# Kernel optimization log

Hardware: AMD Instinct MI355X
Metric: run time of the kernel (lower is better)

## Reference

```python
import jax, jax.numpy as jnp
import numpy as np
from jax import lax

T, D, H, O = 16384, 257, 512, 257


def setup_inputs() -> dict:
    key = jax.random.key(0)
    ks = jax.random.split(key, 7)
    s = 1.0 / np.sqrt(H)  # PyTorch LSTM/Linear uniform init scale
    u = lambda k, shp: jax.random.uniform(k, shp, jnp.float32, -s, s)
    return {
        "stft": jax.random.normal(ks[0], (T, D), jnp.float32),
        "W_ih": u(ks[1], (4 * H, D)),
        "W_hh": u(ks[2], (4 * H, H)),
        "b_ih": u(ks[3], (4 * H,)),
        "b_hh": u(ks[4], (4 * H,)),
        "W_out": u(ks[5], (O, H)),
        "b_out": u(ks[6], (O,)),
    }


def reference(stft, W_ih, W_hh, b_ih, b_hh, W_out, b_out):
    # Batch size is 1 (stft.view(T, 1, -1)), so we scan over [T, D] directly.
    # Precompute input-to-gate GEMM for all timesteps: [T, 4H]
    x_gates = stft @ W_ih.T + (b_ih + b_hh)

    def step(carry, xg):
        h, c = carry  # [H], [H]
        g = xg + h @ W_hh.T  # [4H], PyTorch gate order: i, f, g, o
        i, f, gg, o = jnp.split(g, 4)
        i = jax.nn.sigmoid(i)
        f = jax.nn.sigmoid(f)
        gg = jnp.tanh(gg)
        o = jax.nn.sigmoid(o)
        c = f * c + i * gg
        h = o * jnp.tanh(c)
        return (h, c), h

    h0 = jnp.zeros((H,), stft.dtype)  # init_hidden(): zeros
    c0 = jnp.zeros((H,), stft.dtype)
    _, hs = lax.scan(step, (h0, c0), x_gates)  # hs: [T, H]

    out_space = hs @ W_out.T + b_out  # [T, O]
    return jax.nn.log_softmax(out_space, axis=1)
```

## Files before the change

### kernel.cpp

```cpp
#include <hip/hip_runtime.h>
#include <cmath>

#define T_STEPS 16384
#define D_IN    257
#define H_DIM   512
#define O_DIM   257
#define G4      2048

typedef unsigned long long u64;

#define WS_XG_OFF     8192
#define WS_HS_OFF     (8192 + (size_t)T_STEPS * G4 * 4)

__device__ inline float fast_sigmoid(float x) {
    return 1.f / (1.f + __expf(-x));
}
__device__ inline float fast_tanh(float x) {
    float ax = fminf(fabsf(x), 15.f);
    float e  = __expf(2.f * ax);
    float t  = (e - 1.f) / (e + 1.f);
    return copysignf(t, x);
}
__device__ inline float dot4(float4 a, float4 b) {
    return a.x * b.x + a.y * b.y + a.z * b.z + a.w * b.w;
}

__global__ __launch_bounds__(256) void xgate_gemm(
    const float* __restrict__ stft, const float* __restrict__ W_ih,
    const float* __restrict__ b_ih, const float* __restrict__ b_hh,
    float* __restrict__ xg)
{
    const int tid = threadIdx.x;
    const int tx = tid & 15, ty = tid >> 4;
    const int j0 = blockIdx.x * 64;
    const int t0 = blockIdx.y * 64;

    __shared__ float s_a[64][17];
    __shared__ float s_b[64][17];

    float acc[4][4] = {};

    for (int k0 = 0; k0 < D_IN; k0 += 16) {
        #pragma unroll
        for (int l = 0; l < 4; ++l) {
            int idx = tid + l * 256;
            int r  = idx >> 4;
            int kk = idx & 15;
            int k  = k0 + kk;
            s_a[r][kk] = (k < D_IN) ? stft[(size_t)(t0 + r) * D_IN + k] : 0.f;
            s_b[r][kk] = (k < D_IN) ? W_ih[(size_t)(j0 + r) * D_IN + k] : 0.f;
        }
        __syncthreads();
        #pragma unroll
        for (int kk = 0; kk < 16; ++kk) {
            float a[4], b[4];
            #pragma unroll
            for (int r = 0; r < 4; ++r) a[r] = s_a[ty * 4 + r][kk];
            #pragma unroll
            for (int c = 0; c < 4; ++c) b[c] = s_b[tx * 4 + c][kk];
            #pragma unroll
            for (int r = 0; r < 4; ++r)
                #pragma unroll
                for (int c = 0; c < 4; ++c)
                    acc[r][c] += a[r] * b[c];
        }
        __syncthreads();
    }

    float bias[4];
    #pragma unroll
    for (int c = 0; c < 4; ++c) {
        int j = j0 + tx * 4 + c;
        bias[c] = b_ih[j] + b_hh[j];
    }
    #pragma unroll
    for (int r = 0; r < 4; ++r) {
        int t = t0 + ty * 4 + r;
        #pragma unroll
        for (int c = 0; c < 4; ++c) {
            xg[(size_t)t * G4 + j0 + tx * 4 + c] = acc[r][c] + bias[c];
        }
    }
}

__global__ __launch_bounds__(512, 1) void lstm_seq(
    const float* __restrict__ W_hh, const float* __restrict__ xg,
    float* __restrict__ hs, u64* msg)
{
    const int tid  = threadIdx.x;
    const int g    = blockIdx.x;
    const int w    = tid >> 6;
    const int lane = tid & 63;
    const int j    = lane >> 2;
    const int c    = lane & 3;
    const int colb = w * 64 + c * 16;

    const float* wbase = W_hh + (size_t)(g * 16 + j) * H_DIM + colb;
    const size_t gstride = (size_t)H_DIM * H_DIM;
    float4 wA0, wA1, wA2, wA3, wB0, wB1, wB2, wB3;
    float4 wC0, wC1, wC2, wC3, wD0, wD1, wD2, wD3;
    {
        const float4* p0 = (const float4*)(wbase);
        const float4* p1 = (const float4*)(wbase + gstride);
        const float4* p2 = (const float4*)(wbase + 2 * gstride);
        const float4* p3 = (const float4*)(wbase + 3 * gstride);
        wA0 = p0[0]; wA1 = p0[1]; wA2 = p0[2]; wA3 = p0[3];
        wB0 = p1[0]; wB1 = p1[1]; wB2 = p1[2]; wB3 = p1[3];
        wC0 = p2[0]; wC1 = p2[1]; wC2 = p2[2]; wC3 = p2[3];
        wD0 = p3[0]; wD1 = p3[1]; wD2 = p3[2]; wD3 = p3[3];
    }

    __shared__ float s_h[512];
    __shared__ float s_part[2][512];

    u64* slot0 = msg;
    u64* slot1 = msg + 512;

    float c_state = 0.f;

    const int t_j    = lane & 15;

    for (int t = 0; t < T_STEPS; ++t) {
        const unsigned tagt = (unsigned)t;

        float xv = 0.f;
        if (w == 0) xv = xg[(size_t)t * G4 + (lane >> 4) * H_DIM + g * 16 + t_j];

        u64* rp = ((t & 1) ? slot1 : slot0) + tid;
        u64 u;
        for (;;) {
            u = __hip_atomic_load(rp, __ATOMIC_RELAXED, __HIP_MEMORY_SCOPE_AGENT);
            if ((unsigned)(u >> 32) == tagt) break;
        }

        s_h[tid] = __uint_as_float((unsigned)u);

        const float4* hv = (const float4*)(s_h + colb);
        float4 h0 = hv[0], h1 = hv[1], h2 = hv[2], h3 = hv[3];

        float p0 = dot4(wA0, h0) + dot4(wA1, h1) + dot4(wA2, h2) + dot4(wA3, h3);
        float p1 = dot4(wB0, h0) + dot4(wB1, h1) + dot4(wB2, h2) + dot4(wB3, h3);
        float p2 = dot4(wC0, h0) + dot4(wC1, h1) + dot4(wC2, h2) + dot4(wC3, h3);
        float p3 = dot4(wD0, h0) + dot4(wD1, h1) + dot4(wD2, h2) + dot4(wD3, h3);

        const bool lo2 = (c < 2);
        float a0 = (lo2 ? p0 : p2) + __shfl_xor(lo2 ? p2 : p0, 2, 64);
        float a1 = (lo2 ? p1 : p3) + __shfl_xor(lo2 ? p3 : p1, 2, 64);
        const bool ev = ((c & 1) == 0);
        float fin = (ev ? a0 : a1) + __shfl_xor(ev ? a1 : a0, 1, 64);

        s_part[t & 1][w * 64 + c * 16 + j] = fin;

        asm volatile("s_waitcnt lgkmcnt(0)\n\ts_barrier" ::: "memory");

        if (w == 0) {
            const float* pp = &s_part[t & 1][0];
            float sum = xv;
            #pragma unroll
            for (int k = 0; k < 8; ++k) sum += pp[k * 64 + lane];

            float gi = __shfl(sum, t_j + 0,  64);
            float gf = __shfl(sum, t_j + 16, 64);
            float gg = __shfl(sum, t_j + 32, 64);
            float go = __shfl(sum, t_j + 48, 64);

            float iv = fast_sigmoid(gi);
            float fv = fast_sigmoid(gf);
            float ov = fast_sigmoid(go);
            float gv = fast_tanh(gg);
            c_state = fv * c_state + iv * gv;
            float hn = ov * fast_tanh(c_state);

            if (lane < 16) {
                hs[(size_t)t * H_DIM + g * 16 + lane] = hn;
                u64 m = ((u64)(tagt + 1) << 32) | (u64)__float_as_uint(hn);
                u64* wp = (((t + 1) & 1) ? slot1 : slot0) + (g * 16 + lane);
                __hip_atomic_store(wp, m, __ATOMIC_RELAXED, __HIP_MEMORY_SCOPE_AGENT);
            }
        }
    }
}

__global__ __launch_bounds__(256) void out_softmax(
    const float* __restrict__ hs, const float* __restrict__ W_out,
    const float* __restrict__ b_out, float* __restrict__ out)
{
    const int tid = threadIdx.x;
    const int t0  = blockIdx.x * 16;

    __shared__ float s_w[257 * 33];
    __shared__ float s_hs[16 * 33];
    __shared__ float s_o[16 * 257];
    __shared__ float s_red[8];

    float acc[16] = {};
    float acc256 = 0.f;

    for (int k0 = 0; k0 < H_DIM; k0 += 32) {
        for (int idx = tid; idx < 257 * 32; idx += 256) {
            int row = idx >> 5, col = idx & 31;
            s_w[row * 33 + col] = W_out[(size_t)row * H_DIM + k0 + col];
        }
        for (int idx = tid; idx < 16 * 32; idx += 256) {
            int row = idx >> 5, col = idx & 31;
            s_hs[row * 33 + col] = hs[(size_t)(t0 + row) * H_DIM + k0 + col];
        }
        __syncthreads();
        #pragma unroll
        for (int kk = 0; kk < 32; ++kk) {
            float w = s_w[tid * 33 + kk];
            #pragma unroll
            for (int r = 0; r < 16; ++r)
                acc[r] += s_hs[r * 33 + kk] * w;
        }
        if (tid < 16) {
            #pragma unroll
            for (int kk = 0; kk < 32; ++kk)
                acc256 += s_w[256 * 33 + kk] * s_hs[tid * 33 + kk];
        }
        __syncthreads();
    }

    float bias_c = b_out[tid];
    #pragma unroll
    for (int r = 0; r < 16; ++r) s_o[r * 257 + tid] = acc[r] + bias_c;
    if (tid < 16) s_o[tid * 257 + 256] = acc256 + b_out[256];
    __syncthreads();

    const int lane = tid & 63, wid = tid >> 6;
    for (int r = 0; r < 16; ++r) {
        float v  = s_o[r * 257 + tid];
        float vx = (tid == 0) ? s_o[r * 257 + 256] : -INFINITY;
        float m = fmaxf(v, vx);
        #pragma unroll
        for (int off = 32; off > 0; off >>= 1) m = fmaxf(m, __shfl_xor(m, off, 64));
        if (lane == 0) s_red[wid] = m;
        __syncthreads();
        m = fmaxf(fmaxf(s_red[0], s_red[1]), fmaxf(s_red[2], s_red[3]));
        float e = expf(v - m) + ((tid == 0) ? expf(vx - m) : 0.f);
        #pragma unroll
        for (int off = 32; off > 0; off >>= 1) e += __shfl_xor(e, off, 64);
        if (lane == 0) s_red[4 + wid] = e;
        __syncthreads();
        float s = s_red[4] + s_red[5] + s_red[6] + s_red[7];
        float lg = logf(s) + m;
        out[(size_t)(t0 + r) * O_DIM + tid] = v - lg;
        if (tid == 0) out[(size_t)(t0 + r) * O_DIM + 256] = vx - lg;
    }
}

extern "C" void kernel_launch(void* const* d_in, const int* in_sizes, int n_in,
                              void* d_out, int out_size, void* d_ws, size_t ws_size,
                              hipStream_t stream) {
    (void)in_sizes; (void)n_in; (void)out_size; (void)ws_size;

    const float* stft  = (const float*)d_in[0];
    const float* W_ih  = (const float*)d_in[1];
    const float* W_hh  = (const float*)d_in[2];
    const float* b_ih  = (const float*)d_in[3];
    const float* b_hh  = (const float*)d_in[4];
    const float* W_out = (const float*)d_in[5];
    const float* b_out = (const float*)d_in[6];
    float* out = (float*)d_out;

    char* ws = (char*)d_ws;
    u64* msg  = (u64*)ws;
    float* xg = (float*)(ws + WS_XG_OFF);
    float* hs = (float*)(ws + WS_HS_OFF);

    (void)hipMemsetAsync(ws, 0, 8192, stream);

    xgate_gemm<<<dim3(G4 / 64, T_STEPS / 64), 256, 0, stream>>>(
        stft, W_ih, b_ih, b_hh, xg);
    lstm_seq<<<32, 512, 0, stream>>>(W_hh, xg, hs, msg);
    out_softmax<<<T_STEPS / 16, 256, 0, stream>>>(hs, W_out, b_out, out);
}
```

Before: 27.47 ms.

## Spread LSTM gate epilogue across all warps and prefetch next h message

The post-barrier gate reduction and activation work, previously done by wave 0 alone, is now split across all 8 waves. Each wave reduces partials for 2 hidden units with xor-shuffles and publishes them. A speculative load of the next step's message slot is issued early, so the spin-wait can often finish without a fresh round trip. This shortens the serial critical path per timestep but adds more publishing threads and extra xg loads per wave.

```diff
diff --git a/kernel.cpp b/kernel.cpp
--- a/kernel.cpp
+++ b/kernel.cpp
@@ -116,24 +116,32 @@
     u64* slot0 = msg;
     u64* slot1 = msg + 512;
 
-    float c_state = 0.f;
-
-    const int t_j    = lane & 15;
+    const int rr    = lane >> 3;
+    const int gateT = rr >> 1;
+    const int hhT   = rr & 1;
+    const int rowT  = gateT * 16 + 2 * w + hhT;
+
+    float c_st0 = 0.f, c_st1 = 0.f;
+
+    u64 u_spec = __hip_atomic_load(slot0 + tid, __ATOMIC_RELAXED,
+                                   __HIP_MEMORY_SCOPE_AGENT);
 
     for (int t = 0; t < T_STEPS; ++t) {
         const unsigned tagt = (unsigned)t;
-
-        float xv = 0.f;
-        if (w == 0) xv = xg[(size_t)t * G4 + (lane >> 4) * H_DIM + g * 16 + t_j];
-
-        u64* rp = ((t & 1) ? slot1 : slot0) + tid;
-        u64 u;
-        for (;;) {
+        const int buf = t & 1;
+
+        float xv = xg[(size_t)t * G4 + gateT * H_DIM + g * 16 + 2 * w + hhT];
+
+        u64* rp = (buf ? slot1 : slot0) + tid;
+        u64 u = u_spec;
+        while ((unsigned)(u >> 32) != tagt) {
             u = __hip_atomic_load(rp, __ATOMIC_RELAXED, __HIP_MEMORY_SCOPE_AGENT);
-            if ((unsigned)(u >> 32) == tagt) break;
         }
 
         s_h[tid] = __uint_as_float((unsigned)u);
+
+        u_spec = __hip_atomic_load(((buf ^ 1) ? slot1 : slot0) + tid,
+                                   __ATOMIC_RELAXED, __HIP_MEMORY_SCOPE_AGENT);
 
         const float4* hv = (const float4*)(s_h + colb);
         float4 h0 = hv[0], h1 = hv[1], h2 = hv[2], h3 = hv[3];
@@ -149,34 +157,37 @@
         const bool ev = ((c & 1) == 0);
         float fin = (ev ? a0 : a1) + __shfl_xor(ev ? a1 : a0, 1, 64);
 
-        s_part[t & 1][w * 64 + c * 16 + j] = fin;
+        s_part[buf][w * 64 + c * 16 + j] = fin;
 
         asm volatile("s_waitcnt lgkmcnt(0)\n\ts_barrier" ::: "memory");
 
-        if (w == 0) {
-            const float* pp = &s_part[t & 1][0];
-            float sum = xv;
-            #pragma unroll
-            for (int k = 0; k < 8; ++k) sum += pp[k * 64 + lane];
-
-            float gi = __shfl(sum, t_j + 0,  64);
-            float gf = __shfl(sum, t_j + 16, 64);
-            float gg = __shfl(sum, t_j + 32, 64);
-            float go = __shfl(sum, t_j + 48, 64);
-
-            float iv = fast_sigmoid(gi);
-            float fv = fast_sigmoid(gf);
-            float ov = fast_sigmoid(go);
-            float gv = fast_tanh(gg);
-            c_state = fv * c_state + iv * gv;
-            float hn = ov * fast_tanh(c_state);
-
-            if (lane < 16) {
-                hs[(size_t)t * H_DIM + g * 16 + lane] = hn;
-                u64 m = ((u64)(tagt + 1) << 32) | (u64)__float_as_uint(hn);
-                u64* wp = (((t + 1) & 1) ? slot1 : slot0) + (g * 16 + lane);
-                __hip_atomic_store(wp, m, __ATOMIC_RELAXED, __HIP_MEMORY_SCOPE_AGENT);
-            }
+        float sum = s_part[buf][(lane & 7) * 64 + rowT];
+        sum += __shfl_xor(sum, 1, 64);
+        sum += __shfl_xor(sum, 2, 64);
+        sum += __shfl_xor(sum, 4, 64);
+        float total = sum + xv;
+
+        float gi0 = __shfl(total, 0,  64), gi1 = __shfl(total, 8,  64);
+        float gf0 = __shfl(total, 16, 64), gf1 = __shfl(total, 24, 64);
+        float gg0 = __shfl(total, 32, 64), gg1 = __shfl(total, 40, 64);
+        float go0 = __shfl(total, 48, 64), go1 = __shfl(total, 56, 64);
+
+        float iv0 = fast_sigmoid(gi0), iv1 = fast_sigmoid(gi1);
+        float fv0 = fast_sigmoid(gf0), fv1 = fast_sigmoid(gf1);
+        float ov0 = fast_sigmoid(go0), ov1 = fast_sigmoid(go1);
+        float gv0 = fast_tanh(gg0),    gv1 = fast_tanh(gg1);
+        c_st0 = fv0 * c_st0 + iv0 * gv0;
+        c_st1 = fv1 * c_st1 + iv1 * gv1;
+        float hn0 = ov0 * fast_tanh(c_st0);
+        float hn1 = ov1 * fast_tanh(c_st1);
+
+        if (lane < 2) {
+            float hn = (lane == 0) ? hn0 : hn1;
+            const int hidx = g * 16 + 2 * w + lane;
+            hs[(size_t)t * H_DIM + hidx] = hn;
+            u64 m = ((u64)(tagt + 1) << 32) | (u64)__float_as_uint(hn);
+            u64* wp = (((t + 1) & 1) ? slot1 : slot0) + hidx;
+            __hip_atomic_store(wp, m, __ATOMIC_RELAXED, __HIP_MEMORY_SCOPE_AGENT);
         }
     }
 }
```

Result: slower. 46.00 ms (+67.4%).
